# Kernel tuning notes

Hardware: AMD Instinct MI355X
Metric: run time of the kernel (lower is better)

Reference implementation:

```python
import jax, jax.numpy as jnp
import numpy as np
from math import factorial

# ----- hyperparams (mirror init_kwargs) -----
HIDDEN = [(32,0,1),(32,0,-1),(8,1,1),(8,1,-1),(4,2,1),(4,2,-1)]  # (mul, l, parity)
SCALAR = [(32,0,1)]
SH_IRR = [(1,0,1),(1,1,-1),(1,2,1)]  # spherical harmonics 0e+1o+2e
EMB, NUM_RBF, R_MAX, MLP_DIM, D_IN = 32, 16, 10.0, 256, 64
N_NODES, N_EDGES, N_GRAPHS = 2048, 8192, 8
EDGE_FEATS_DIM = NUM_RBF + 2*EMB

def _slices(irs):
    s, o = [], 0
    for m, l, _ in irs:
        s.append(o); o += m*(2*l+1)
    return s

def _su2_cg(j1, j2, j3, m1, m2, m3):
    if m1 + m2 != m3:
        return 0.0
    f = factorial
    pref = ((2*j3+1)*f(j3+j1-j2)*f(j3-j1+j2)*f(j1+j2-j3)/f(j1+j2+j3+1))**0.5
    pref *= (f(j3+m3)*f(j3-m3)*f(j1-m1)*f(j1+m1)*f(j2-m2)*f(j2+m2))**0.5
    s = 0.0
    for k in range(0, j1+j2-j3+1):
        if j1-m1-k < 0 or j2+m2-k < 0 or j3-j2+m1+k < 0 or j3-j1-m2+k < 0:
            continue
        s += (-1.0)**k/(f(k)*f(j1+j2-j3-k)*f(j1-m1-k)*f(j2+m2-k)*f(j3-j2+m1+k)*f(j3-j1-m2+k))
    return pref*s

def _q(l):  # real -> complex change of basis (e3nn convention incl. (-i)^l phase)
    q = np.zeros((2*l+1, 2*l+1), dtype=np.complex128)
    for m in range(-l, 0):
        q[l+m, l+abs(m)] = 2**-0.5
        q[l+m, l-abs(m)] = -1j*2**-0.5
    q[l, l] = 1.0
    for m in range(1, l+1):
        q[l+m, l+abs(m)] = (-1)**m*2**-0.5
        q[l+m, l-abs(m)] = 1j*(-1)**m*2**-0.5
    return (-1j)**l*q

def _real_cg(l1, l2, l3):  # real-basis Clebsch-Gordan, unit Frobenius norm (wigner-3j-like)
    C = np.zeros((2*l1+1, 2*l2+1, 2*l3+1), dtype=np.complex128)
    for m1 in range(-l1, l1+1):
        for m2 in range(-l2, l2+1):
            m3 = m1 + m2
            if abs(m3) <= l3:
                C[l1+m1, l2+m2, l3+m3] = _su2_cg(l1, l2, l3, m1, m2, m3)
    w = np.einsum('ai,bj,ck,abc->ijk', _q(l1), _q(l2), np.conj(_q(l3)), C)
    re, im = np.real(w), np.imag(w)
    w = re if np.linalg.norm(re) >= np.linalg.norm(im) else im
    return (w/np.linalg.norm(w)).astype(np.float32)

_CG = {}
def cg(l1, l2, l3):
    if (l1, l2, l3) not in _CG:
        _CG[(l1, l2, l3)] = jnp.asarray(_real_cg(l1, l2, l3))
    return _CG[(l1, l2, l3)]

def _build_layer(ir_in, ir_out):  # FullyConnectedTensorProduct path enumeration
    si = _slices(ir_in)
    paths, woff, fan = [], 0, [0]*len(ir_out)
    for i1, (m1, l1, p1) in enumerate(ir_in):
        for (_, l2, p2) in SH_IRR:
            for i3, (m3, l3, p3) in enumerate(ir_out):
                if p1*p2 == p3 and abs(l1-l2) <= l3 <= l1+l2:
                    paths.append((si[i1], m1, l1, l2, i3, m3, l3, woff))
                    fan[i3] += m1
                    woff += m1*m3
    return paths, woff, fan, ir_out

L_SPECS = [_build_layer(SCALAR, HIDDEN), _build_layer(HIDDEN, HIDDEN),
           _build_layer(HIDDEN, HIDDEN), _build_layer(HIDDEN, SCALAR)]
W_NUMELS = [s[1] for s in L_SPECS]  # [1408, 4320, 4320, 1408]

def spherical_harmonics(u):  # component-normalized real SH, l=0,1,2, on unit vectors
    xc, yc, zc = u[:, 0], u[:, 1], u[:, 2]
    s3, s15, s5 = 3**0.5, 15**0.5, 5**0.5
    return jnp.stack([jnp.ones_like(xc),
                      s3*yc, s3*zc, s3*xc,
                      s15*xc*yc, s15*yc*zc, s5*0.5*(3*zc*zc-1.0), s15*xc*zc,
                      s15*0.5*(xc*xc-yc*yc)], axis=1)

def tp_messages(x, sh, w, spec):  # per-edge equivariant tensor product with edge-dep weights
    paths, _, fan, ir_out = spec
    E = x.shape[0]
    outs = [jnp.zeros((E, m*(2*l+1)), x.dtype) for m, l, _ in ir_out]
    for (o1, m1, l1, l2, i3, m3, l3, woff) in paths:
        xp = x[:, o1:o1+m1*(2*l1+1)].reshape(E, m1, 2*l1+1)
        shp = sh[:, l2*l2:(l2+1)*(l2+1)]
        wp = w[:, woff:woff+m1*m3].reshape(E, m1, m3)
        alpha = float(np.sqrt((2*l3+1)/fan[i3]))  # component/element path normalization
        y = alpha*jnp.einsum('eui,ej,euv,ijk->evk', xp, shp, wp, cg(l1, l2, l3))
        outs[i3] = outs[i3] + y.reshape(E, -1)
    return jnp.concatenate(outs, axis=1)

def batch_norm(h, ir_out, eps=1e-5):  # e3nn-style equivariant batch norm (train stats, identity affine)
    outs, o = [], 0
    for m, l, _ in ir_out:
        d = m*(2*l+1)
        f = h[:, o:o+d].reshape(-1, m, 2*l+1); o += d
        if l == 0:
            f = f - f.mean(axis=0, keepdims=True)
        norm2 = (f*f).mean(axis=(0, 2), keepdims=True)
        outs.append((f*jax.lax.rsqrt(norm2+eps)).reshape(h.shape[0], -1))
    return jnp.concatenate(outs, axis=1)

def scatter_mean(msg, idx, n):
    s = jax.ops.segment_sum(msg, idx, num_segments=n)
    c = jax.ops.segment_sum(jnp.ones((idx.shape[0], 1), msg.dtype), idx, num_segments=n)
    return s/jnp.maximum(c, 1.0)

def _forward(x, pos, edge_index, batch, emb_w, emb_b, layer_params):
    ei = jnp.concatenate([edge_index, edge_index[::-1]], axis=1)  # to_undirected (both directions)
    src, dst = ei[0], ei[1]
    h = x@emb_w + emb_b  # (N, 32)
    vec = pos[src] - pos[dst]
    lengths = jnp.linalg.norm(vec, axis=-1)
    sh = spherical_harmonics(vec/lengths[:, None])  # (E, 9)
    mu = jnp.linspace(0.0, R_MAX, NUM_RBF)
    sigma = R_MAX/NUM_RBF
    rbf = jnp.exp(-(((lengths[:, None]-mu)/sigma)**2))  # (E, 16)
    for li, (w1, b1, w2, b2) in enumerate(layer_params):
        ef = jnp.concatenate([rbf, h[src, :EMB], h[dst, :EMB]], axis=1)  # (E, 80)
        w = jax.nn.relu(ef@w1 + b1)@w2 + b2  # per-edge TP weights (dropout=eval noop)
        upd = scatter_mean(tp_messages(h[dst], sh, w, L_SPECS[li]), src, N_NODES)
        upd = batch_norm(upd, L_SPECS[li][3])
        d = upd.shape[-1]
        h_res = h[:, :d] if h.shape[-1] >= d else jnp.pad(h, ((0, 0), (0, d-h.shape[-1])))
        h = upd + h_res  # residual with pad/truncate (F.pad semantics)
    graph = jax.ops.segment_sum(h, batch, num_segments=N_GRAPHS)
    return h, graph

def setup_inputs():
    key = jax.random.key(0)
    ks = jax.random.split(key, 32)
    inp = {}
    inp['x'] = jax.random.normal(ks[0], (N_NODES, D_IN), jnp.float32)
    inp['pos'] = 3.0*jax.random.normal(ks[1], (N_NODES, 3), jnp.float32)
    s = jax.random.randint(ks[2], (N_EDGES,), 0, N_NODES)
    d = (s + jax.random.randint(ks[3], (N_EDGES,), 1, N_NODES)) % N_NODES  # no self-loops
    inp['edge_index'] = jnp.stack([s, d]).astype(jnp.int32)
    inp['batch'] = jnp.sort(jax.random.randint(ks[4], (N_NODES,), 0, N_GRAPHS)).astype(jnp.int32)
    inp['emb_w'] = jax.random.normal(ks[5], (D_IN, EMB), jnp.float32)/np.sqrt(D_IN)
    inp['emb_b'] = jnp.zeros((EMB,), jnp.float32)
    k = 6
    for i, wn in enumerate(W_NUMELS):
        inp[f'l{i}_w1'] = jax.random.normal(ks[k], (EDGE_FEATS_DIM, MLP_DIM), jnp.float32)/np.sqrt(EDGE_FEATS_DIM); k += 1
        inp[f'l{i}_b1'] = jnp.zeros((MLP_DIM,), jnp.float32)
        inp[f'l{i}_w2'] = jax.random.normal(ks[k], (MLP_DIM, wn), jnp.float32)/np.sqrt(MLP_DIM); k += 1
        inp[f'l{i}_b2'] = jnp.zeros((wn,), jnp.float32)
    return inp

def reference(x, pos, edge_index, batch, emb_w, emb_b,
              l0_w1, l0_b1, l0_w2, l0_b2, l1_w1, l1_b1, l1_w2, l1_b2,
              l2_w1, l2_b1, l2_w2, l2_b2, l3_w1, l3_b1, l3_w2, l3_b2):
    lp = [(l0_w1, l0_b1, l0_w2, l0_b2), (l1_w1, l1_b1, l1_w2, l1_b2),
          (l2_w1, l2_b1, l2_w2, l2_b2), (l3_w1, l3_b1, l3_w2, l3_b2)]
    return _forward(x, pos, edge_index, batch, emb_w, emb_b, lp)
```

## Files before the change

### kernel.cpp

```cpp
#include <hip/hip_runtime.h>
#include <hip/hip_bf16.h>
#include <math.h>

#define NNODES 2048
#define NEDG   8192
#define E2     16384
#define NGRAPH 8
#define HSTR   152

static const int LD_DIN[4]  = {32,152,152,152};
static const int LD_DOUT[4] = {152,152,152,32};
static const int LD_WN[4]   = {1408,4320,4320,1408};
static const int LD_WNP[4]  = {1408,4352,4352,1408};
static const int LD_NCH[4]  = {88,88,88,32};
static const int LD_RES[4]  = {32,152,152,152};
#define WNP_MAX 4352

#define SLOT_MAX    1088
#define CELL_N      20
#define SEG_S_N     164
#define SEG_ENT_MAX 1024

typedef short bf16x8 __attribute__((ext_vector_type(8)));
typedef float f32x4  __attribute__((ext_vector_type(4)));

constexpr double cfact(int n){ double r=1.0; for(int i=2;i<=n;i++) r*=(double)i; return r; }
constexpr double csqrt(double x){
  if(x<=0.0) return 0.0;
  double g = x>1.0? x:1.0;
  for(int i=0;i<64;i++) g=0.5*(g+x/g);
  return g;
}
constexpr double csu2cg(int j1,int j2,int j3,int m1,int m2,int m3){
  if(m1+m2!=m3) return 0.0;
  double pref = csqrt((double)(2*j3+1)*cfact(j3+j1-j2)*cfact(j3-j1+j2)*cfact(j1+j2-j3)/cfact(j1+j2+j3+1));
  pref *= csqrt(cfact(j3+m3)*cfact(j3-m3)*cfact(j1-m1)*cfact(j1+m1)*cfact(j2-m2)*cfact(j2+m2));
  double s=0.0;
  for(int k=0;k<=j1+j2-j3;k++){
    if(j1-m1-k<0||j2+m2-k<0||j3-j2+m1+k<0||j3-j1-m2+k<0) continue;
    double t=1.0/(cfact(k)*cfact(j1+j2-j3-k)*cfact(j1-m1-k)*cfact(j2+m2-k)*cfact(j3-j2+m1+k)*cfact(j3-j1-m2+k));
    s += (k&1)? -t : t;
  }
  return pref*s;
}
struct QM { double r[25]; double i[25]; };
constexpr QM cqmat(int l){
  QM q{};
  const double inv2=0.7071067811865476;
  for(int m=-l;m<0;m++){
    int am=-m;
    q.r[(l+m)*5+(l+am)] = inv2;
    q.i[(l+m)*5+(l-am)] = -inv2;
  }
  q.r[l*5+l]=1.0;
  for(int m=1;m<=l;m++){
    double sgn=(m&1)? -1.0:1.0;
    q.r[(l+m)*5+(l+m)] = sgn*inv2;
    q.i[(l+m)*5+(l-m)] = sgn*inv2;
  }
  for(int rep=0;rep<l;rep++){
    for(int t=0;t<25;t++){ double a=q.r[t], b=q.i[t]; q.r[t]=b; q.i[t]=-a; }
  }
  return q;
}
struct CGCell { float v[125]; };
constexpr CGCell mkcell(int l1,int l2,int l3){
  CGCell out{};
  int lo = l1>l2? l1-l2 : l2-l1;
  if(l3<lo || l3>l1+l2) return out;
  QM q1=cqmat(l1), q2=cqmat(l2), q3=cqmat(l3);
  int n1=2*l1+1,n2=2*l2+1,n3=2*l3+1;
  double C[125]={};
  for(int a=0;a<n1;a++)for(int b=0;b<n2;b++)for(int c=0;c<n3;c++)
    C[a*25+b*5+c]=csu2cg(l1,l2,l3,a-l1,b-l2,c-l3);
  double wr[125]={}, wi[125]={};
  for(int i=0;i<n1;i++)for(int j=0;j<n2;j++)for(int k=0;k<n3;k++){
    double ar=0.0, ai=0.0;
    for(int a=0;a<n1;a++)for(int b=0;b<n2;b++){
      double p1r=q1.r[a*5+i], p1i=q1.i[a*5+i];
      double p2r=q2.r[b*5+j], p2i=q2.i[b*5+j];
      double pr=p1r*p2r-p1i*p2i, pi=p1r*p2i+p1i*p2r;
      for(int c=0;c<n3;c++){
        double cv=C[a*25+b*5+c]; if(cv==0.0) continue;
        double p3r=q3.r[c*5+k], p3i=-q3.i[c*5+k];
        ar += (pr*p3r-pi*p3i)*cv;
        ai += (pr*p3i+pi*p3r)*cv;
      }
    }
    wr[i*25+j*5+k]=ar; wi[i*25+j*5+k]=ai;
  }
  double sr=0.0, si=0.0;
  for(int t=0;t<125;t++){ sr+=wr[t]*wr[t]; si+=wi[t]*wi[t]; }
  double nr=csqrt(sr), ni=csqrt(si);
  bool use_re = nr>=ni;
  double nn = use_re? nr:ni;
  double inv = (nn>1e-300)? 1.0/nn : 0.0;
  for(int t=0;t<125;t++) out.v[t]=(float)((use_re? wr[t]:wi[t])*inv);
  return out;
}
constexpr CGCell CGc0 =mkcell(0,0,0), CGc1 =mkcell(0,0,1), CGc2 =mkcell(0,0,2);
constexpr CGCell CGc3 =mkcell(0,1,0), CGc4 =mkcell(0,1,1), CGc5 =mkcell(0,1,2);
constexpr CGCell CGc6 =mkcell(0,2,0), CGc7 =mkcell(0,2,1), CGc8 =mkcell(0,2,2);
constexpr CGCell CGc9 =mkcell(1,0,0), CGc10=mkcell(1,0,1), CGc11=mkcell(1,0,2);
constexpr CGCell CGc12=mkcell(1,1,0), CGc13=mkcell(1,1,1), CGc14=mkcell(1,1,2);
constexpr CGCell CGc15=mkcell(1,2,0), CGc16=mkcell(1,2,1), CGc17=mkcell(1,2,2);
constexpr CGCell CGc18=mkcell(2,0,0), CGc19=mkcell(2,0,1), CGc20=mkcell(2,0,2);
constexpr CGCell CGc21=mkcell(2,1,0), CGc22=mkcell(2,1,1), CGc23=mkcell(2,1,2);
constexpr CGCell CGc24=mkcell(2,2,0), CGc25=mkcell(2,2,1), CGc26=mkcell(2,2,2);
__constant__ CGCell g_cg[27] = {
  CGc0,CGc1,CGc2,CGc3,CGc4,CGc5,CGc6,CGc7,CGc8,
  CGc9,CGc10,CGc11,CGc12,CGc13,CGc14,CGc15,CGc16,CGc17,
  CGc18,CGc19,CGc20,CGc21,CGc22,CGc23,CGc24,CGc25,CGc26};

#define MAXP 32
struct LayerSpec {
  int np, zc, wn, nc;
  int x_off[MAXP], m1[MAXP], d1[MAXP], sh_off[MAXP], d2[MAXP], d3[MAXP],
      m3[MAXP], woff[MAXP], out_sl[MAXP], cg_idx[MAXP], zbase[MAXP], cell[MAXP];
  float alpha[MAXP];
  int cellcg[16];
};
constexpr LayerSpec mkspec(int li){
  LayerSpec S{};
  const int IRH[6][3]={{32,0,1},{32,0,-1},{8,1,1},{8,1,-1},{4,2,1},{4,2,-1}};
  const int IRS[1][3]={{32,0,1}};
  const int SH2[3][2]={{0,1},{1,-1},{2,1}};
  const int (*irin)[3]  = (li==0)? IRS: IRH; int nin =(li==0)?1:6;
  const int (*irout)[3] = (li==3)? IRS: IRH; int nout=(li==3)?1:6;
  int si_in[6]={}, si_out[6]={};
  { int o=0; for(int i=0;i<nin;i++){ si_in[i]=o;  o+=irin[i][0]*(2*irin[i][1]+1);} }
  { int o=0; for(int i=0;i<nout;i++){ si_out[i]=o; o+=irout[i][0]*(2*irout[i][1]+1);} }
  int fan[6]={};
  int i3a[MAXP]={};
  int np=0, woff=0, zb=0, nc=0;
  for(int i1=0;i1<nin;i1++){
    int m1=irin[i1][0], l1=irin[i1][1], p1=irin[i1][2];
    for(int s=0;s<3;s++){
      int l2=SH2[s][0], p2=SH2[s][1];
      for(int i3=0;i3<nout;i3++){
        int m3=irout[i3][0], l3=irout[i3][1], p3=irout[i3][2];
        int lo = l1>l2? l1-l2 : l2-l1;
        if(p1*p2==p3 && l3>=lo && l3<=l1+l2){
          S.x_off[np]=si_in[i1]; S.m1[np]=m1; S.d1[np]=2*l1+1;
          S.sh_off[np]=l2*l2; S.d2[np]=2*l2+1; S.d3[np]=2*l3+1;
          S.m3[np]=m3; S.woff[np]=woff; S.out_sl[np]=si_out[i3];
          S.cg_idx[np]=l1*9+l2*3+l3; S.zbase[np]=zb;
          int ci=-1;
          for(int c=0;c<nc;c++) if(S.cellcg[c]==S.cg_idx[np]) ci=c;
          if(ci<0){ S.cellcg[nc]=S.cg_idx[np]; ci=nc++; }
          S.cell[np]=ci; i3a[np]=i3;
          np++;
          fan[i3]+=m1; woff+=m1*m3; zb+=m1*(2*l3+1);
        }
      }
    }
  }
  for(int p=0;p<np;p++)
    S.alpha[p]=(float)csqrt((double)(2*((S.d3[p]-1)/2)+1)/(double)fan[i3a[p]]);
  S.np=np; S.zc=zb; S.wn=woff; S.nc=nc;
  return S;
}
constexpr LayerSpec LS0=mkspec(0), LS1=mkspec(1), LS2=mkspec(2), LS3=mkspec(3);
__constant__ LayerSpec g_spec[4]={LS0,LS1,LS2,LS3};

__global__ __launch_bounds__(256) void build_tables_kernel(
    unsigned* __restrict__ slot_tab, unsigned* __restrict__ cell_tab,
    int* __restrict__ seg_start, unsigned* __restrict__ seg_ent,
    int* __restrict__ perm, float* __restrict__ alpha_col){
  __shared__ int vals[256];
  __shared__ int part[256];
  int tid=threadIdx.x;
  int li=blockIdx.x;
  const LayerSpec& S=g_spec[li];
  int np=S.np, zc=S.zc, nc=S.nc, wn=S.wn;
  for(int c=tid;c<nc;c+=256){
    int cgi=S.cellcg[c];
    int l2=(cgi/3)%3;
    cell_tab[li*CELL_N+c]=(unsigned)cgi | ((unsigned)(l2*l2)<<8) | ((unsigned)(2*l2+1)<<12);
  }
  for(int s=tid;s<zc;s+=256){
    int p=0; while(p+1<np && S.zbase[p+1]<=s) p++;
    int rel=s-S.zbase[p];
    int k=rel/S.m1[p], u=rel-k*S.m1[p];
    slot_tab[li*SLOT_MAX+s]=(unsigned)(S.x_off[p]+u*S.d1[p]) | ((unsigned)k<<9) | ((unsigned)S.cell[p]<<12);
  }
  int* pm=perm+li*WNP_MAX;
  float* ac=alpha_col+li*WNP_MAX;
  for(int j=tid;j<wn;j+=256){
    int p=0; while(p+1<np && S.woff[p+1]<=j) p++;
    int rel=j-S.woff[p];
    int v=rel/S.m1[p], u=rel%S.m1[p];
    pm[j]=S.woff[p]+u*S.m3[p]+v;
    ac[j]=S.alpha[p];
  }
  int Dout=(li==3)?32:152;
  for(int d=tid;d<Dout;d+=256){
    int cnt=0;
    for(int p=0;p<np;p++){
      int rel=d-S.out_sl[p];
      if(rel>=0 && rel<S.m3[p]*S.d3[p]) cnt++;
    }
    vals[d]=cnt;
  }
  __syncthreads();
  int v0=(tid<Dout)? vals[tid]:0;
  part[tid]=v0;
  __syncthreads();
  for(int ofs=1;ofs<256;ofs<<=1){
    int v=(tid>=ofs)? part[tid-ofs]:0;
    __syncthreads();
    part[tid]+=v;
    __syncthreads();
  }
  int* sst=seg_start+li*SEG_S_N;
  if(tid<Dout) sst[tid]=part[tid]-v0;
  if(tid==0) sst[Dout]=part[255];
  __syncthreads();
  unsigned* se=seg_ent+li*SEG_ENT_MAX;
  for(int d=tid;d<Dout;d+=256){
    int pos=sst[d];
    for(int p=0;p<np;p++){
      int rel=d-S.out_sl[p];
      if(rel>=0 && rel<S.m3[p]*S.d3[p]){
        int v=rel/S.d3[p], k=rel%S.d3[p];
        unsigned z0=(unsigned)(S.zbase[p]+k*S.m1[p]);
        unsigned w0=(unsigned)(S.woff[p]+v*S.m1[p]);
        unsigned code=(S.m1[p]==32)?2u:((S.m1[p]==8)?1u:0u);
        se[pos]= z0 | (w0<<11) | (code<<24);
        pos++;
      }
    }
  }
}

__global__ void geom_kernel(const float* __restrict__ pos, const int* __restrict__ ei,
                            int* __restrict__ src2, int* __restrict__ dst2,
                            float* __restrict__ sh, float* __restrict__ rbf,
                            int* __restrict__ counts){
  int e=blockIdx.x*256+threadIdx.x;
  if(e>=E2) return;
  int s,d;
  if(e<NEDG){ s=ei[e]; d=ei[NEDG+e]; }
  else { int j=e-NEDG; s=ei[NEDG+j]; d=ei[j]; }
  src2[e]=s; dst2[e]=d;
  atomicAdd(&counts[s],1);
  float vx=pos[s*3+0]-pos[d*3+0];
  float vy=pos[s*3+1]-pos[d*3+1];
  float vz=pos[s*3+2]-pos[d*3+2];
  float len=sqrtf(vx*vx+vy*vy+vz*vz);
  float inv=1.f/len;
  float x=vx*inv, y=vy*inv, z=vz*inv;
  const float s3=1.7320508075688772f, s15=3.872983346207417f, s5=2.23606797749979f;
  float* shp=sh+(size_t)e*9;
  shp[0]=1.f; shp[1]=s3*y; shp[2]=s3*z; shp[3]=s3*x;
  shp[4]=s15*x*y; shp[5]=s15*y*z; shp[6]=s5*0.5f*(3.f*z*z-1.f);
  shp[7]=s15*x*z; shp[8]=s15*0.5f*(x*x-y*y);
  float* rp=rbf+(size_t)e*16;
  const float invsig=1.6f;
  for(int k=0;k<16;k++){
    float t=(len-(10.0f/15.0f)*(float)k)*invsig;
    rp[k]=expf(-t*t);
  }
}

__global__ void scan_kernel(const int* __restrict__ counts, int* __restrict__ row_ptr){
  __shared__ int part[256];
  int t=threadIdx.x;
  int base=t*8;
  int loc[8]; int s=0;
  #pragma unroll
  for(int i=0;i<8;i++){ loc[i]=counts[base+i]; s+=loc[i]; }
  part[t]=s; __syncthreads();
  for(int ofs=1; ofs<256; ofs<<=1){
    int v=(t>=ofs)? part[t-ofs]:0;
    __syncthreads();
    part[t]+=v;
    __syncthreads();
  }
  int run=part[t]-s;
  #pragma unroll
  for(int i=0;i<8;i++){ row_ptr[base+i]=run; run+=loc[i]; }
  if(t==255) row_ptr[NNODES]=run;
}

__global__ void csr_fill_kernel(const int* __restrict__ src2, const int* __restrict__ row_ptr,
                                int* __restrict__ cursor, int* __restrict__ eidx){
  int e=blockIdx.x*256+threadIdx.x;
  if(e>=E2) return;
  int s=src2[e];
  int p=atomicAdd(&cursor[s],1);
  eidx[row_ptr[s]+p]=e;
}

__global__ void embed_kernel(const float* __restrict__ x, const float* __restrict__ W,
                             const float* __restrict__ b, float* __restrict__ h){
  int idx=blockIdx.x*256+threadIdx.x;
  int n=idx>>5, j=idx&31;
  float acc=b[j];
  for(int k=0;k<64;k++) acc += x[n*64+k]*W[k*32+j];
  h[(size_t)n*HSTR+j]=acc;
}

__global__ void cast_w2t_kernel(const float* __restrict__ w2, const int* __restrict__ perm,
                                const float* __restrict__ alpha_col,
                                __hip_bfloat16* __restrict__ w2t, int wn, int wn_pad){
  int idx=blockIdx.x*256+threadIdx.x;
  if(idx>=wn_pad*256) return;
  int j=idx>>8, k=idx&255;
  float v=(j<wn)? w2[(size_t)k*wn+perm[j]]*alpha_col[j] : 0.f;
  w2t[idx]=__float2bfloat16(v);
}

__global__ __launch_bounds__(256) void mlp1_kernel(
    const float* __restrict__ h, const float* __restrict__ rbf,
    const int* __restrict__ src2, const int* __restrict__ dst2,
    const float* __restrict__ w1, const float* __restrict__ b1,
    __hip_bfloat16* __restrict__ hidden, int e_start){
  __shared__ float ef[16][80];
  int tid=threadIdx.x;
  int e0=e_start+blockIdx.x*16;
  for(int t=tid;t<16*80;t+=256){
    int el=t/80, k=t-el*80; int ge=e0+el;
    float v;
    if(k<16)      v=rbf[(size_t)ge*16+k];
    else if(k<48) v=h[(size_t)src2[ge]*HSTR+(k-16)];
    else          v=h[(size_t)dst2[ge]*HSTR+(k-48)];
    ef[el][k]=v;
  }
  __syncthreads();
  float acc[16];
  float bv=b1[tid];
  #pragma unroll
  for(int e=0;e<16;e++) acc[e]=bv;
  for(int k=0;k<80;k++){
    float wv=w1[k*256+tid];
    #pragma unroll
    for(int e=0;e<16;e++) acc[e]+=ef[e][k]*wv;
  }
  int le0=blockIdx.x*16;
  #pragma unroll
  for(int e=0;e<16;e++)
    hidden[(size_t)(le0+e)*256+tid]=__float2bfloat16(fmaxf(acc[e],0.f));
}

__global__ __launch_bounds__(256) void mlp2_mfma_kernel(
    const __hip_bfloat16* __restrict__ hidden,
    const __hip_bfloat16* __restrict__ w2t,
    const float* __restrict__ b2, const int* __restrict__ perm,
    const float* __restrict__ alpha_col,
    __hip_bfloat16* __restrict__ wbuf, int wn, int wn_pad){
  __shared__ __hip_bfloat16 As[128*32];
  __shared__ __hip_bfloat16 Bs[128*32];
  int tid=threadIdx.x;
  int lane=tid&63;
  int m0=blockIdx.x*128, n0=blockIdx.y*128;
  int mw=((tid>>6)&1)*64, nw=(tid>>7)*64;
  f32x4 acc[4][4];
  #pragma unroll
  for(int i=0;i<4;i++)
    #pragma unroll
    for(int j=0;j<4;j++) acc[i][j]=(f32x4){0.f,0.f,0.f,0.f};

  int i0=tid*8, i1=tid*8+2048;
  int ar0=i0>>5, ac0=i0&31, ar1=i1>>5, ac1=i1&31;
  const int q4=lane>>4, c16=lane&15;

  for(int k0=0;k0<256;k0+=32){
    __syncthreads();
    *(uint4*)&As[ar0*32+ac0] = *(const uint4*)&hidden[(size_t)(m0+ar0)*256 + k0 + ac0];
    *(uint4*)&As[ar1*32+ac1] = *(const uint4*)&hidden[(size_t)(m0+ar1)*256 + k0 + ac1];
    *(uint4*)&Bs[ar0*32+ac0] = *(const uint4*)&w2t[(size_t)(n0+ar0)*256 + k0 + ac0];
    *(uint4*)&Bs[ar1*32+ac1] = *(const uint4*)&w2t[(size_t)(n0+ar1)*256 + k0 + ac1];
    __syncthreads();
    bf16x8 af[4], bfr[4];
    #pragma unroll
    for(int mi=0;mi<4;mi++) af[mi]=*(bf16x8*)&As[(mw+mi*16+c16)*32 + q4*8];
    #pragma unroll
    for(int ni=0;ni<4;ni++) bfr[ni]=*(bf16x8*)&Bs[(nw+ni*16+c16)*32 + q4*8];
    #pragma unroll
    for(int mi=0;mi<4;mi++)
      #pragma unroll
      for(int ni=0;ni<4;ni++)
        acc[mi][ni]=__builtin_amdgcn_mfma_f32_16x16x32_bf16(af[mi],bfr[ni],acc[mi][ni],0,0,0);
  }
  #pragma unroll
  for(int ni=0;ni<4;ni++){
    int col=n0+nw+ni*16+c16;
    float bias=(col<wn)? b2[perm[col]]*alpha_col[col]:0.f;
    #pragma unroll
    for(int mi=0;mi<4;mi++){
      int row=m0+mw+mi*16+q4*4;
      #pragma unroll
      for(int rr=0;rr<4;rr++)
        wbuf[(size_t)(row+rr)*wn_pad+col]=__float2bfloat16(acc[mi][ni][rr]+bias);
    }
  }
}

__device__ inline void wave_sync(){
  __builtin_amdgcn_s_waitcnt(0);
  __builtin_amdgcn_wave_barrier();
}

__device__ inline float dot8f(const float* zp, const __hip_bfloat16* wp){
  f32x4 za=*(const f32x4*)zp;
  f32x4 zb=*(const f32x4*)(zp+4);
  uint4 wv=*(const uint4*)wp;
  const __hip_bfloat16* wl=(const __hip_bfloat16*)&wv;
  float s=0.f;
  #pragma unroll
  for(int t=0;t<4;t++) s+=za[t]*__bfloat162float(wl[t]);
  #pragma unroll
  for(int t=0;t<4;t++) s+=zb[t]*__bfloat162float(wl[4+t]);
  return s;
}
__device__ inline float dot4f(const float* zp, const __hip_bfloat16* wp){
  f32x4 za=*(const f32x4*)zp;
  uint2 wv=*(const uint2*)wp;
  const __hip_bfloat16* wl=(const __hip_bfloat16*)&wv;
  float s=0.f;
  #pragma unroll
  for(int t=0;t<4;t++) s+=za[t]*__bfloat162float(wl[t]);
  return s;
}

__global__ __launch_bounds__(256) void tp4_kernel(
    const float* __restrict__ h, const float* __restrict__ sh,
    const __hip_bfloat16* __restrict__ wbuf, const int* __restrict__ dst2,
    const unsigned* __restrict__ slot_tab, const unsigned* __restrict__ cell_tab,
    const int* __restrict__ seg_start, const unsigned* __restrict__ seg_ent,
    float* __restrict__ msg, int e_start, int Din, int Dout, int wstride,
    int zc, int nc){
  __shared__ float xrow[4][160];
  __shared__ float shs[4][12];
  __shared__ float zsm[4][1088];
  __shared__ float Tw[4][376];
  int tid=threadIdx.x, w=tid>>6, lane=tid&63;
  int le=blockIdx.x*4+w, ge=e_start+le;
  int dn=dst2[ge];
  for(int i=lane;i<Din;i+=64) xrow[w][i]=h[(size_t)dn*HSTR+i];
  for(int i=Din+lane;i<160;i+=64) xrow[w][i]=0.f;
  if(lane<9) shs[w][lane]=sh[(size_t)ge*9+lane];
  wave_sync();
  float* T=&Tw[w][0];
  for(int t=lane;t<nc*25;t+=64){
    int c=t/25, r=t-c*25, k=r/5, i=r-k*5;
    unsigned cm=cell_tab[c];
    int cgi=cm&255, sho=(cm>>8)&15, d2=(cm>>12)&7;
    const float* cgp=g_cg[cgi].v + i*25 + k;
    float s=0.f;
    for(int j=0;j<d2;j++) s+=cgp[j*5]*shs[w][sho+j];
    T[t]=s;
  }
  wave_sync();
  const float* xr=&xrow[w][0];
  for(int s=lane;s<zc;s+=64){
    unsigned st=slot_tab[s];
    int xb=st&511, k=(st>>9)&7, c=st>>12;
    const float* Tp=&T[c*25+k*5];
    zsm[w][s]=xr[xb]*Tp[0]+xr[xb+1]*Tp[1]+xr[xb+2]*Tp[2]+xr[xb+3]*Tp[3]+xr[xb+4]*Tp[4];
  }
  wave_sync();
  const __hip_bfloat16* wrow=wbuf+(size_t)le*wstride;
  const float* zbase=&zsm[w][0];
  for(int d=lane;d<Dout;d+=64){
    int s0=seg_start[d], s1=seg_start[d+1];
    float acc=0.f;
    for(int s=s0;s<s1;s++){
      unsigned sg=seg_ent[s];
      int z0=sg&2047, w0=(sg>>11)&8191, code=sg>>24;
      const float* zp=zbase+z0;
      const __hip_bfloat16* wp=wrow+w0;
      if(code==2){
        #pragma unroll
        for(int t=0;t<4;t++) acc+=dot8f(zp+t*8,wp+t*8);
      } else if(code==1){
        acc+=dot8f(zp,wp);
      } else {
        acc+=dot4f(zp,wp);
      }
    }
    msg[(size_t)ge*Dout+d]=acc;
  }
}

__global__ void aggregate_kernel(const float* __restrict__ msg, const int* __restrict__ row_ptr,
                                 const int* __restrict__ eidx, const int* __restrict__ counts,
                                 float* __restrict__ upd, int Dout){
  int n=blockIdx.x; int lane=threadIdx.x;
  int p0=row_ptr[n], p1=row_ptr[n+1];
  int c=counts[n]; if(c<1) c=1;
  float inv=1.f/(float)c;
  for(int d=lane;d<Dout;d+=64){
    float s=0.f;
    for(int p=p0;p<p1;p++) s+=msg[(size_t)eidx[p]*Dout+d];
    upd[(size_t)n*Dout+d]=s*inv;
  }
}

__device__ inline int hidden_chan_of_dim(int d){
  if(d<64)  return d;
  if(d<88)  return 64+(d-64)/3;
  if(d<112) return 72+(d-88)/3;
  if(d<132) return 80+(d-112)/5;
  return 84+(d-132)/5;
}
__device__ inline void hidden_chan_params(int c, int& off, int& dk, int& l0){
  if(c<64){ off=c; dk=1; l0=1; }
  else if(c<72){ off=64+(c-64)*3; dk=3; l0=0; }
  else if(c<80){ off=88+(c-72)*3; dk=3; l0=0; }
  else if(c<84){ off=112+(c-80)*5; dk=5; l0=0; }
  else { off=132+(c-84)*5; dk=5; l0=0; }
}

__global__ void stats_kernel(const float* __restrict__ upd, float* __restrict__ stats,
                             int Dout, int scalar_out){
  int c=blockIdx.x, tid=threadIdx.x;
  int off,dk,l0;
  if(scalar_out){ off=c; dk=1; l0=1; }
  else hidden_chan_params(c,off,dk,l0);
  float s=0.f, s2=0.f;
  int total=NNODES*dk;
  for(int t=tid;t<total;t+=256){
    int n=t/dk, k=t-n*dk;
    float v=upd[(size_t)n*Dout+off+k];
    s+=v; s2+=v*v;
  }
  __shared__ float rs[256], rs2[256];
  rs[tid]=s; rs2[tid]=s2; __syncthreads();
  for(int o=128;o>0;o>>=1){
    if(tid<o){ rs[tid]+=rs[tid+o]; rs2[tid]+=rs2[tid+o]; }
    __syncthreads();
  }
  if(tid==0){
    float cnt=(float)total;
    float mean = l0? rs[0]/cnt : 0.f;
    float var = rs2[0]/cnt - mean*mean;
    stats[c*2]=mean;
    stats[c*2+1]=1.0f/sqrtf(var+1e-5f);
  }
}

__global__ void apply_kernel(const float* __restrict__ upd, const float* __restrict__ stats,
                             const float* __restrict__ h_cur, float* __restrict__ h_next,
                             int Dout, int res_dim, int scalar_out, int out_stride){
  int idx=blockIdx.x*256+threadIdx.x;
  if(idx>=NNODES*Dout) return;
  int n=idx/Dout, d=idx-n*Dout;
  int c = scalar_out? d : hidden_chan_of_dim(d);
  float v=(upd[idx]-stats[2*c])*stats[2*c+1];
  float res=(d<res_dim)? h_cur[(size_t)n*HSTR+d] : 0.f;
  h_next[(size_t)n*out_stride+d]=v+res;
}

__global__ void graph_kernel(const float* __restrict__ hfin, const int* __restrict__ batch,
                             float* __restrict__ gout){
  int idx=blockIdx.x*256+threadIdx.x;
  int n=idx>>5, d=idx&31;
  atomicAdd(&gout[batch[n]*32+d], hfin[idx]);
}

extern "C" void kernel_launch(void* const* d_in, const int* in_sizes, int n_in,
                              void* d_out, int out_size, void* d_ws, size_t ws_size,
                              hipStream_t stream){
  (void)in_sizes; (void)n_in; (void)out_size;
  const float* x    =(const float*)d_in[0];
  const float* pos  =(const float*)d_in[1];
  const int*   ei   =(const int*)d_in[2];
  const int*   batch=(const int*)d_in[3];
  const float* emb_w=(const float*)d_in[4];
  const float* emb_b=(const float*)d_in[5];
  const float *W1[4], *B1[4], *W2[4], *B2[4];
  for(int l=0;l<4;l++){
    W1[l]=(const float*)d_in[6+4*l];
    B1[l]=(const float*)d_in[7+4*l];
    W2[l]=(const float*)d_in[8+4*l];
    B2[l]=(const float*)d_in[9+4*l];
  }
  int ZC[4]={LS0.zc,LS1.zc,LS2.zc,LS3.zc};
  int NC[4]={LS0.nc,LS1.nc,LS2.nc,LS3.nc};

  char* base=(char*)d_ws;
  size_t off=0;
  auto alloc=[&](size_t bytes)->char*{
    off=(off+255)&~(size_t)255;
    char* p=base+off; off+=bytes; return p;
  };
  float*  h_a   =(float*)alloc((size_t)NNODES*HSTR*4);
  float*  h_b   =(float*)alloc((size_t)NNODES*HSTR*4);
  float*  shb   =(float*)alloc((size_t)E2*9*4);
  float*  rbfb  =(float*)alloc((size_t)E2*16*4);
  int*    src2  =(int*)  alloc((size_t)E2*4);
  int*    dst2  =(int*)  alloc((size_t)E2*4);
  int*    counts=(int*)  alloc((size_t)NNODES*4);
  int*    cursor=(int*)  alloc((size_t)NNODES*4);
  int*    row_ptr=(int*) alloc((size_t)(NNODES+4)*4);
  int*    eidx  =(int*)  alloc((size_t)E2*4);
  float*  msg   =(float*)alloc((size_t)E2*HSTR*4);
  float*  upd   =(float*)alloc((size_t)NNODES*HSTR*4);
  float*  stats =(float*)alloc(256*4);
  unsigned* slot_tab=(unsigned*)alloc((size_t)4*SLOT_MAX*4);
  unsigned* cell_tg =(unsigned*)alloc((size_t)4*CELL_N*4);
  int*      seg_s   =(int*)     alloc((size_t)4*SEG_S_N*4);
  unsigned* seg_e   =(unsigned*)alloc((size_t)4*SEG_ENT_MAX*4);
  int*      perm    =(int*)     alloc((size_t)4*WNP_MAX*4);
  float*    alpha_c =(float*)   alloc((size_t)4*WNP_MAX*4);
  __hip_bfloat16* w2t[4];
  for(int l=0;l<4;l++) w2t[l]=(__hip_bfloat16*)alloc((size_t)LD_WNP[l]*256*2);

  int E_CHUNK=E2;
  while(E_CHUNK>128){
    size_t need=off;
    need=(need+255)&~(size_t)255; need+=(size_t)E_CHUNK*256*2;
    need=(need+255)&~(size_t)255; need+=(size_t)E_CHUNK*WNP_MAX*2;
    if(need<=ws_size) break;
    E_CHUNK>>=1;
  }
  __hip_bfloat16* hidden=(__hip_bfloat16*)alloc((size_t)E_CHUNK*256*2);
  __hip_bfloat16* wbuf  =(__hip_bfloat16*)alloc((size_t)E_CHUNK*WNP_MAX*2);

  hipMemsetAsync(counts,0,(size_t)NNODES*4,stream);
  hipMemsetAsync(cursor,0,(size_t)NNODES*4,stream);
  build_tables_kernel<<<4,256,0,stream>>>(slot_tab,cell_tg,seg_s,seg_e,perm,alpha_c);
  geom_kernel<<<E2/256,256,0,stream>>>(pos,ei,src2,dst2,shb,rbfb,counts);
  scan_kernel<<<1,256,0,stream>>>(counts,row_ptr);
  csr_fill_kernel<<<E2/256,256,0,stream>>>(src2,row_ptr,cursor,eidx);
  embed_kernel<<<(NNODES*32)/256,256,0,stream>>>(x,emb_w,emb_b,h_a);
  for(int l=0;l<4;l++)
    cast_w2t_kernel<<<(LD_WNP[l]*256+255)/256,256,0,stream>>>(
        W2[l],perm+l*WNP_MAX,alpha_c+l*WNP_MAX,w2t[l],LD_WN[l],LD_WNP[l]);

  float* h_cur=h_a; float* h_nxt=h_b;
  for(int li=0;li<4;li++){
    int wn=LD_WN[li], wnp=LD_WNP[li], Din=LD_DIN[li], Dout=LD_DOUT[li];
    for(int e0=0;e0<E2;e0+=E_CHUNK){
      mlp1_kernel<<<E_CHUNK/16,256,0,stream>>>(h_cur,rbfb,src2,dst2,W1[li],B1[li],hidden,e0);
      dim3 g2(E_CHUNK/128, wnp/128);
      mlp2_mfma_kernel<<<g2,256,0,stream>>>(hidden,w2t[li],B2[li],perm+li*WNP_MAX,
                                            alpha_c+li*WNP_MAX,wbuf,wn,wnp);
      tp4_kernel<<<E_CHUNK/4,256,0,stream>>>(h_cur,shb,wbuf,dst2,
          slot_tab+li*SLOT_MAX, cell_tg+li*CELL_N,
          seg_s+li*SEG_S_N, seg_e+li*SEG_ENT_MAX,
          msg,e0,Din,Dout,wnp, ZC[li], NC[li]);
    }
    aggregate_kernel<<<NNODES,64,0,stream>>>(msg,row_ptr,eidx,counts,upd,Dout);
    stats_kernel<<<LD_NCH[li],256,0,stream>>>(upd,stats,Dout,li==3?1:0);
    int tot=NNODES*Dout;
    if(li<3)
      apply_kernel<<<(tot+255)/256,256,0,stream>>>(upd,stats,h_cur,h_nxt,Dout,LD_RES[li],0,HSTR);
    else
      apply_kernel<<<(tot+255)/256,256,0,stream>>>(upd,stats,h_cur,(float*)d_out,Dout,LD_RES[li],1,32);
    float* tmp=h_cur; h_cur=h_nxt; h_nxt=tmp;
  }

  float* gout=(float*)d_out + (size_t)NNODES*32;
  hipMemsetAsync(gout,0,(size_t)NGRAPH*32*4,stream);
  graph_kernel<<<(NNODES*32)/256,256,0,stream>>>((const float*)d_out,batch,gout);
}
```

Before: 808.0 us.

## Fuse edge aggregation into tensor-product kernel with atomic scatter-add

The tensor-product kernel now atomically adds each edge message straight into the per-node update buffer. This removes the per-edge message buffer, the CSR build (scan and fill kernels) and the separate aggregate kernel. Mean normalisation moves into the stats and apply kernels through a precomputed inverse-count array. In exchange it adds float atomics, which may contend on high-degree nodes and make the summation order non-deterministic, plus a memset of the update buffer for each layer.

```diff
diff --git a/kernel.cpp b/kernel.cpp
--- a/kernel.cpp
+++ b/kernel.cpp
@@ -263,33 +263,11 @@
   }
 }
 
-__global__ void scan_kernel(const int* __restrict__ counts, int* __restrict__ row_ptr){
-  __shared__ int part[256];
-  int t=threadIdx.x;
-  int base=t*8;
-  int loc[8]; int s=0;
-  #pragma unroll
-  for(int i=0;i<8;i++){ loc[i]=counts[base+i]; s+=loc[i]; }
-  part[t]=s; __syncthreads();
-  for(int ofs=1; ofs<256; ofs<<=1){
-    int v=(t>=ofs)? part[t-ofs]:0;
-    __syncthreads();
-    part[t]+=v;
-    __syncthreads();
-  }
-  int run=part[t]-s;
-  #pragma unroll
-  for(int i=0;i<8;i++){ row_ptr[base+i]=run; run+=loc[i]; }
-  if(t==255) row_ptr[NNODES]=run;
-}
-
-__global__ void csr_fill_kernel(const int* __restrict__ src2, const int* __restrict__ row_ptr,
-                                int* __restrict__ cursor, int* __restrict__ eidx){
-  int e=blockIdx.x*256+threadIdx.x;
-  if(e>=E2) return;
-  int s=src2[e];
-  int p=atomicAdd(&cursor[s],1);
-  eidx[row_ptr[s]+p]=e;
+__global__ void invc_kernel(const int* __restrict__ counts, float* __restrict__ invc){
+  int n=blockIdx.x*256+threadIdx.x;
+  if(n>=NNODES) return;
+  int c=counts[n]; if(c<1) c=1;
+  invc[n]=1.f/(float)c;
 }
 
 __global__ void embed_kernel(const float* __restrict__ x, const float* __restrict__ W,
@@ -426,10 +404,11 @@
 
 __global__ __launch_bounds__(256) void tp4_kernel(
     const float* __restrict__ h, const float* __restrict__ sh,
-    const __hip_bfloat16* __restrict__ wbuf, const int* __restrict__ dst2,
+    const __hip_bfloat16* __restrict__ wbuf,
+    const int* __restrict__ src2, const int* __restrict__ dst2,
     const unsigned* __restrict__ slot_tab, const unsigned* __restrict__ cell_tab,
     const int* __restrict__ seg_start, const unsigned* __restrict__ seg_ent,
-    float* __restrict__ msg, int e_start, int Din, int Dout, int wstride,
+    float* __restrict__ upd, int e_start, int Din, int Dout, int wstride,
     int zc, int nc){
   __shared__ float xrow[4][160];
   __shared__ float shs[4][12];
@@ -438,6 +417,7 @@
   int tid=threadIdx.x, w=tid>>6, lane=tid&63;
   int le=blockIdx.x*4+w, ge=e_start+le;
   int dn=dst2[ge];
+  int sn=src2[ge];
   for(int i=lane;i<Din;i+=64) xrow[w][i]=h[(size_t)dn*HSTR+i];
   for(int i=Din+lane;i<160;i+=64) xrow[w][i]=0.f;
   if(lane<9) shs[w][lane]=sh[(size_t)ge*9+lane];
@@ -463,6 +443,7 @@
   wave_sync();
   const __hip_bfloat16* wrow=wbuf+(size_t)le*wstride;
   const float* zbase=&zsm[w][0];
+  float* urow=upd+(size_t)sn*Dout;
   for(int d=lane;d<Dout;d+=64){
     int s0=seg_start[d], s1=seg_start[d+1];
     float acc=0.f;
@@ -480,21 +461,7 @@
         acc+=dot4f(zp,wp);
       }
     }
-    msg[(size_t)ge*Dout+d]=acc;
-  }
-}
-
-__global__ void aggregate_kernel(const float* __restrict__ msg, const int* __restrict__ row_ptr,
-                                 const int* __restrict__ eidx, const int* __restrict__ counts,
-                                 float* __restrict__ upd, int Dout){
-  int n=blockIdx.x; int lane=threadIdx.x;
-  int p0=row_ptr[n], p1=row_ptr[n+1];
-  int c=counts[n]; if(c<1) c=1;
-  float inv=1.f/(float)c;
-  for(int d=lane;d<Dout;d+=64){
-    float s=0.f;
-    for(int p=p0;p<p1;p++) s+=msg[(size_t)eidx[p]*Dout+d];
-    upd[(size_t)n*Dout+d]=s*inv;
+    atomicAdd(&urow[d], acc);
   }
 }
 
@@ -513,8 +480,8 @@
   else { off=132+(c-84)*5; dk=5; l0=0; }
 }
 
-__global__ void stats_kernel(const float* __restrict__ upd, float* __restrict__ stats,
-                             int Dout, int scalar_out){
+__global__ void stats_kernel(const float* __restrict__ upd, const float* __restrict__ invc,
+                             float* __restrict__ stats, int Dout, int scalar_out){
   int c=blockIdx.x, tid=threadIdx.x;
   int off,dk,l0;
   if(scalar_out){ off=c; dk=1; l0=1; }
@@ -523,7 +490,7 @@
   int total=NNODES*dk;
   for(int t=tid;t<total;t+=256){
     int n=t/dk, k=t-n*dk;
-    float v=upd[(size_t)n*Dout+off+k];
+    float v=upd[(size_t)n*Dout+off+k]*invc[n];
     s+=v; s2+=v*v;
   }
   __shared__ float rs[256], rs2[256];
@@ -541,14 +508,15 @@
   }
 }
 
-__global__ void apply_kernel(const float* __restrict__ upd, const float* __restrict__ stats,
+__global__ void apply_kernel(const float* __restrict__ upd, const float* __restrict__ invc,
+                             const float* __restrict__ stats,
                              const float* __restrict__ h_cur, float* __restrict__ h_next,
                              int Dout, int res_dim, int scalar_out, int out_stride){
   int idx=blockIdx.x*256+threadIdx.x;
   if(idx>=NNODES*Dout) return;
   int n=idx/Dout, d=idx-n*Dout;
   int c = scalar_out? d : hidden_chan_of_dim(d);
-  float v=(upd[idx]-stats[2*c])*stats[2*c+1];
+  float v=(upd[idx]*invc[n]-stats[2*c])*stats[2*c+1];
   float res=(d<res_dim)? h_cur[(size_t)n*HSTR+d] : 0.f;
   h_next[(size_t)n*out_stride+d]=v+res;
 }
@@ -593,10 +561,7 @@
   int*    src2  =(int*)  alloc((size_t)E2*4);
   int*    dst2  =(int*)  alloc((size_t)E2*4);
   int*    counts=(int*)  alloc((size_t)NNODES*4);
-  int*    cursor=(int*)  alloc((size_t)NNODES*4);
-  int*    row_ptr=(int*) alloc((size_t)(NNODES+4)*4);
-  int*    eidx  =(int*)  alloc((size_t)E2*4);
-  float*  msg   =(float*)alloc((size_t)E2*HSTR*4);
+  float*  invc  =(float*)alloc((size_t)NNODES*4);
   float*  upd   =(float*)alloc((size_t)NNODES*HSTR*4);
   float*  stats =(float*)alloc(256*4);
   unsigned* slot_tab=(unsigned*)alloc((size_t)4*SLOT_MAX*4);
@@ -620,11 +585,9 @@
   __hip_bfloat16* wbuf  =(__hip_bfloat16*)alloc((size_t)E_CHUNK*WNP_MAX*2);
 
   hipMemsetAsync(counts,0,(size_t)NNODES*4,stream);
-  hipMemsetAsync(cursor,0,(size_t)NNODES*4,stream);
   build_tables_kernel<<<4,256,0,stream>>>(slot_tab,cell_tg,seg_s,seg_e,perm,alpha_c);
   geom_kernel<<<E2/256,256,0,stream>>>(pos,ei,src2,dst2,shb,rbfb,counts);
-  scan_kernel<<<1,256,0,stream>>>(counts,row_ptr);
-  csr_fill_kernel<<<E2/256,256,0,stream>>>(src2,row_ptr,cursor,eidx);
+  invc_kernel<<<NNODES/256,256,0,stream>>>(counts,invc);
   embed_kernel<<<(NNODES*32)/256,256,0,stream>>>(x,emb_w,emb_b,h_a);
   for(int l=0;l<4;l++)
     cast_w2t_kernel<<<(LD_WNP[l]*256+255)/256,256,0,stream>>>(
@@ -633,23 +596,23 @@
   float* h_cur=h_a; float* h_nxt=h_b;
   for(int li=0;li<4;li++){
     int wn=LD_WN[li], wnp=LD_WNP[li], Din=LD_DIN[li], Dout=LD_DOUT[li];
+    hipMemsetAsync(upd,0,(size_t)NNODES*Dout*4,stream);
     for(int e0=0;e0<E2;e0+=E_CHUNK){
       mlp1_kernel<<<E_CHUNK/16,256,0,stream>>>(h_cur,rbfb,src2,dst2,W1[li],B1[li],hidden,e0);
       dim3 g2(E_CHUNK/128, wnp/128);
       mlp2_mfma_kernel<<<g2,256,0,stream>>>(hidden,w2t[li],B2[li],perm+li*WNP_MAX,
                                             alpha_c+li*WNP_MAX,wbuf,wn,wnp);
-      tp4_kernel<<<E_CHUNK/4,256,0,stream>>>(h_cur,shb,wbuf,dst2,
+      tp4_kernel<<<E_CHUNK/4,256,0,stream>>>(h_cur,shb,wbuf,src2,dst2,
           slot_tab+li*SLOT_MAX, cell_tg+li*CELL_N,
           seg_s+li*SEG_S_N, seg_e+li*SEG_ENT_MAX,
-          msg,e0,Din,Dout,wnp, ZC[li], NC[li]);
+          upd,e0,Din,Dout,wnp, ZC[li], NC[li]);
     }
-    aggregate_kernel<<<NNODES,64,0,stream>>>(msg,row_ptr,eidx,counts,upd,Dout);
-    stats_kernel<<<LD_NCH[li],256,0,stream>>>(upd,stats,Dout,li==3?1:0);
+    stats_kernel<<<LD_NCH[li],256,0,stream>>>(upd,invc,stats,Dout,li==3?1:0);
     int tot=NNODES*Dout;
     if(li<3)
-      apply_kernel<<<(tot+255)/256,256,0,stream>>>(upd,stats,h_cur,h_nxt,Dout,LD_RES[li],0,HSTR);
+      apply_kernel<<<(tot+255)/256,256,0,stream>>>(upd,invc,stats,h_cur,h_nxt,Dout,LD_RES[li],0,HSTR);
     else
-      apply_kernel<<<(tot+255)/256,256,0,stream>>>(upd,stats,h_cur,(float*)d_out,Dout,LD_RES[li],1,32);
+      apply_kernel<<<(tot+255)/256,256,0,stream>>>(upd,invc,stats,h_cur,(float*)d_out,Dout,LD_RES[li],1,32);
     float* tmp=h_cur; h_cur=h_nxt; h_nxt=tmp;
   }
 
```

Result: faster. 756.4 us (-6.4%).
